# Kernel optimization log

Hardware: AMD Instinct MI355X
Metric: run time of the kernel (lower is better)

## Reference

```python
import jax, jax.numpy as jnp
import numpy as np

N, E, D, DFF, OUT = 50000, 800000, 128, 256, 119
NUM_MASK = 7500

def setup_inputs() -> dict:
    key = jax.random.key(0)
    ks = jax.random.split(key, 12)
    return {
        "x": jax.random.normal(ks[0], (N, D), jnp.float32),
        "edge_index": jax.random.randint(ks[1], (2, E), 0, N, jnp.int64),
        "edge_attr": jax.random.randint(ks[2], (E, 2), 0, 3, jnp.int64),
        "masked_idx": jax.random.randint(ks[3], (NUM_MASK,), 0, N, jnp.int64),
        "prelu_a": jnp.float32(0.25),
        "W_enc": jax.random.normal(ks[4], (D, D), jnp.float32) * (1.0 / np.sqrt(D)),
        "emb1": jax.random.normal(ks[5], (6, D), jnp.float32) * 0.1,
        "emb2": jax.random.normal(ks[6], (3, D), jnp.float32) * 0.1,
        "W1": jax.random.normal(ks[7], (DFF, D), jnp.float32) * (1.0 / np.sqrt(D)),
        "b1": jnp.zeros((DFF,), jnp.float32),
        "W2": jax.random.normal(ks[8], (OUT, DFF), jnp.float32) * (1.0 / np.sqrt(DFF)),
        "b2": jnp.zeros((OUT,), jnp.float32),
    }

def reference(x, edge_index, edge_attr, masked_idx, prelu_a, W_enc, emb1, emb2, W1, b1, W2, b2):
    n = x.shape[0]
    # PReLU -> enc_to_dec (no bias) -> zero masked nodes
    h = jnp.where(x > 0, x, prelu_a * x)
    h = h @ W_enc.T
    h = h.at[masked_idx].set(0.0)
    # add self loops (self-loop edge_attr = [4, 0])
    loop = jnp.arange(n, dtype=edge_index.dtype)
    src = jnp.concatenate([edge_index[0], loop])
    dst = jnp.concatenate([edge_index[1], loop])
    et = jnp.concatenate([edge_attr[:, 0], jnp.full((n,), 4, edge_attr.dtype)])
    ed = jnp.concatenate([edge_attr[:, 1], jnp.zeros((n,), edge_attr.dtype)])
    edge_emb = emb1[et] + emb2[ed]          # [E+N, D]
    msg = h[src] + edge_emb                 # gather + add
    aggr = jax.ops.segment_sum(msg, dst, num_segments=n)  # scatter-add
    # GIN MLP update
    hid = jax.nn.relu(aggr @ W1.T + b1)
    return hid @ W2.T + b2
```

## Files before the change

### kernel.cpp

```cpp
#include <hip/hip_runtime.h>
#include <hip/hip_fp16.h>


typedef unsigned long long ull;
typedef _Float16 half8 __attribute__((ext_vector_type(8)));
typedef float    f32x4 __attribute__((ext_vector_type(4)));

#define MFMA16(a, b, c) __builtin_amdgcn_mfma_f32_16x16x32_f16(a, b, c, 0, 0, 0)
#define BCAP 4608
#define EPB  2048

__global__ __launch_bounds__(256) void k_wconv(const float* __restrict__ Wen,
                                               const float* __restrict__ W1,
                                               const float* __restrict__ W2,
                                               __half* __restrict__ Wen16,
                                               __half* __restrict__ W1_16,
                                               __half* __restrict__ W2_16p,
                                               int* __restrict__ gcur)
{
    int i = blockIdx.x * 256 + threadIdx.x;
    if (blockIdx.x == 0) gcur[threadIdx.x] = 0;
    if (i < 128 * 128) Wen16[i] = __float2half(Wen[i]);
    if (i < 256 * 128) W1_16[i] = __float2half(W1[i]);
    if (i < 128 * 256) {
        int r = i >> 8;
        W2_16p[i] = (r < 119) ? __float2half(W2[i]) : __half(0.0f);
    }
}

__device__ __forceinline__ half8 prelu_h8(const float* __restrict__ p, float a)
{
    float4 v0 = *(const float4*)p;
    float4 v1 = *(const float4*)(p + 4);
    half8 r;
    r[0] = (_Float16)(v0.x > 0.f ? v0.x : a * v0.x);
    r[1] = (_Float16)(v0.y > 0.f ? v0.y : a * v0.y);
    r[2] = (_Float16)(v0.z > 0.f ? v0.z : a * v0.z);
    r[3] = (_Float16)(v0.w > 0.f ? v0.w : a * v0.w);
    r[4] = (_Float16)(v1.x > 0.f ? v1.x : a * v1.x);
    r[5] = (_Float16)(v1.y > 0.f ? v1.y : a * v1.y);
    r[6] = (_Float16)(v1.z > 0.f ? v1.z : a * v1.z);
    r[7] = (_Float16)(v1.w > 0.f ? v1.w : a * v1.w);
    return r;
}

__global__ __launch_bounds__(256) void k_pre(const float* __restrict__ x,
                                             const __half* __restrict__ Wen16,
                                             const float* __restrict__ prelu_a,
                                             __half* __restrict__ h16,
                                             const int* __restrict__ ei,
                                             const int* __restrict__ ea,
                                             int* __restrict__ gcur,
                                             unsigned int* __restrict__ binned,
                                             int n, int E, int nbEnc, int nbBin)
{
    __shared__ __half Wel[128 * 136];
    __shared__ int lcnt[256];
    int t = threadIdx.x;

    if ((int)blockIdx.x >= nbEnc) {
        int b = blockIdx.x - nbEnc;
        int e0 = b * EPB;
        lcnt[t] = 0;
        __syncthreads();
        unsigned int rec[8];
        int bk[8];
#pragma unroll
        for (int u = 0; u < 8; ++u) {
            int e = e0 + u * 256 + t;
            if (e < E) {
                int src = ei[e];
                int dst = ei[E + e];
                int et  = ea[2 * e];
                int ed  = ea[2 * e + 1];
                rec[u] = (unsigned int)src | ((unsigned int)et << 17)
                       | ((unsigned int)ed << 19)
                       | ((unsigned int)(dst & 255) << 21);
                bk[u] = dst >> 8;
                atomicAdd(&lcnt[bk[u]], 1);
            } else bk[u] = -1;
        }
        __syncthreads();
        int c = lcnt[t];
        lcnt[t] = (c > 0) ? atomicAdd(&gcur[t], c) : 0;
        __syncthreads();
#pragma unroll
        for (int u = 0; u < 8; ++u) {
            if (bk[u] >= 0) {
                int pos = atomicAdd(&lcnt[bk[u]], 1);
                if (pos < BCAP) binned[(size_t)bk[u] * BCAP + pos] = rec[u];
            }
        }
        return;
    }

    for (int c = t; c < 2048; c += 256) {
        int row = c >> 4, slot = c & 15;
        *(uint4*)((char*)Wel + row * 272 + slot * 16) =
            *(const uint4*)((const char*)Wen16 + (size_t)c * 16);
    }
    __syncthreads();
    int lane = t & 63, wid = t >> 6;
    int rowbase = blockIdx.x * 128 + wid * 32;
    int mr0 = min(rowbase + (lane & 15), n - 1);
    int mr1 = min(rowbase + 16 + (lane & 15), n - 1);
    int kg = (lane >> 4) * 8, slotb = lane >> 4;
    float a = prelu_a[0];
    f32x4 acc[16] = {};
#pragma unroll
    for (int ks = 0; ks < 4; ++ks) {
        half8 a0 = prelu_h8(x + ((size_t)mr0 << 7) + ks * 32 + kg, a);
        half8 a1 = prelu_h8(x + ((size_t)mr1 << 7) + ks * 32 + kg, a);
        const char* wp = (const char*)Wel + (size_t)(lane & 15) * 272
                       + (ks * 4 + slotb) * 16;
#pragma unroll
        for (int ct = 0; ct < 8; ++ct) {
            half8 bf = *(const half8*)(wp + ct * (16 * 272));
            acc[ct * 2]     = MFMA16(a0, bf, acc[ct * 2]);
            acc[ct * 2 + 1] = MFMA16(a1, bf, acc[ct * 2 + 1]);
        }
    }
#pragma unroll
    for (int ct = 0; ct < 8; ++ct)
#pragma unroll
        for (int h = 0; h < 2; ++h)
#pragma unroll
            for (int r = 0; r < 4; ++r) {
                int node = rowbase + h * 16 + ((lane >> 4) << 2) + r;
                if (node < n)
                    h16[((size_t)node << 7) + (ct << 4) + (lane & 15)] =
                        __float2half(acc[ct * 2 + h][r]);
            }
}

__global__ void k_mask(const int* __restrict__ midx,
                       unsigned int* __restrict__ h16u, int nm)
{
    int idx = blockIdx.x * blockDim.x + threadIdx.x;
    if (idx >= nm * 64) return;
    int m = idx >> 6, l = idx & 63;
    h16u[(((size_t)midx[m]) << 6) + l] = 0u;
}

__global__ __launch_bounds__(256) void k_bucket(const unsigned int* __restrict__ binned,
                                                const int* __restrict__ gcur,
                                                ull* __restrict__ cnt64,
                                                int* __restrict__ off,
                                                int* __restrict__ sorted,
                                                int n, int nb)
{
    __shared__ ull lc[256];
    __shared__ int sg[2][256];
    __shared__ int curs[256];
    int b = blockIdx.x >> 1, half = blockIdx.x & 1;
    int t = threadIdx.x;

    int gv = (t < nb) ? min(gcur[t], BCAP) : 0;
    sg[0][t] = gv;
    lc[t] = 0;
    __syncthreads();
    int cb = 0;
    for (int d = 1; d < 256; d <<= 1) {
        int v = sg[cb][t];
        if (t >= d) v += sg[cb][t - d];
        sg[cb ^ 1][t] = v;
        cb ^= 1;
        __syncthreads();
    }
    int ebase = (b == 0) ? 0 : sg[cb][b - 1];
    int mcnt = min(gcur[b], BCAP);
    __syncthreads();

    const unsigned int* bp = binned + (size_t)b * BCAP;
    for (int i = t; i < mcnt; i += 256) {
        unsigned int rec = bp[i];
        int dl = (rec >> 21) & 255;
        int et = (rec >> 17) & 3;
        int ed = (rec >> 19) & 3;
        atomicAdd(&lc[dl], (1ULL << (10 * et)) | (1ULL << (30 + 10 * ed)));
    }
    __syncthreads();

    ull c = lc[t];
    int deg = (int)((c & 1023) + ((c >> 10) & 1023) + ((c >> 20) & 1023));
    sg[0][t] = deg;
    __syncthreads();
    cb = 0;
    for (int d = 1; d < 256; d <<= 1) {
        int v = sg[cb][t];
        if (t >= d) v += sg[cb][t - d];
        sg[cb ^ 1][t] = v;
        cb ^= 1;
        __syncthreads();
    }
    int loc = sg[cb][t] - deg;
    int dst = (b << 8) + t;
    if (dst < n && (t >> 7) == half) {
        cnt64[dst] = c;
        off[dst]   = ebase + loc;
    }
    curs[t] = ebase + loc;
    __syncthreads();

    for (int i = t; i < mcnt; i += 256) {
        unsigned int rec = bp[i];
        int dl = (rec >> 21) & 255;
        if ((dl >> 7) != half) continue;
        int p = atomicAdd(&curs[dl], 1);
        sorted[p] = (int)(rec & 0x1FFFF);
    }
}

__global__ __launch_bounds__(256) void k_agg(const uint2* __restrict__ h16u2,
                                             const int* __restrict__ off,
                                             const ull* __restrict__ cnt64,
                                             const int* __restrict__ sorted,
                                             const float* __restrict__ emb1,
                                             const float* __restrict__ emb2,
                                             uint2* __restrict__ aggr16u2,
                                             int n)
{
    int t = threadIdx.x;
    int l32 = t & 31;
    int node = blockIdx.x * 8 + (t >> 5);
    if (node >= n) return;
    int p = l32 << 2;
    float4 E10 = *(const float4*)(emb1 + 0 * 128 + p);
    float4 E11 = *(const float4*)(emb1 + 1 * 128 + p);
    float4 E12 = *(const float4*)(emb1 + 2 * 128 + p);
    float4 E14 = *(const float4*)(emb1 + 4 * 128 + p);
    float4 E20 = *(const float4*)(emb2 + 0 * 128 + p);
    float4 E21 = *(const float4*)(emb2 + 1 * 128 + p);
    float4 E22 = *(const float4*)(emb2 + 2 * 128 + p);

    ull c = cnt64[node];
    float c0 = (float)(c & 1023), c1 = (float)((c >> 10) & 1023),
          c2 = (float)((c >> 20) & 1023);
    float d0 = (float)((c >> 30) & 1023), d1 = (float)((c >> 40) & 1023),
          d2 = (float)((c >> 50) & 1023);
    int deg = (int)(c & 1023) + (int)((c >> 10) & 1023) + (int)((c >> 20) & 1023);

    uint2 hv = h16u2[(size_t)node * 32 + l32];
    float2 hA = __half22float2(*(__half2*)&hv.x);
    float2 hB = __half22float2(*(__half2*)&hv.y);
    float4 base;
    base.x = hA.x + E14.x + E20.x;
    base.y = hA.y + E14.y + E20.y;
    base.z = hB.x + E14.z + E20.z;
    base.w = hB.y + E14.w + E20.w;
    base.x = fmaf(c0, E10.x, fmaf(c1, E11.x, fmaf(c2, E12.x, base.x)));
    base.y = fmaf(c0, E10.y, fmaf(c1, E11.y, fmaf(c2, E12.y, base.y)));
    base.z = fmaf(c0, E10.z, fmaf(c1, E11.z, fmaf(c2, E12.z, base.z)));
    base.w = fmaf(c0, E10.w, fmaf(c1, E11.w, fmaf(c2, E12.w, base.w)));
    base.x = fmaf(d0, E20.x, fmaf(d1, E21.x, fmaf(d2, E22.x, base.x)));
    base.y = fmaf(d0, E20.y, fmaf(d1, E21.y, fmaf(d2, E22.y, base.y)));
    base.z = fmaf(d0, E20.z, fmaf(d1, E21.z, fmaf(d2, E22.z, base.z)));
    base.w = fmaf(d0, E20.w, fmaf(d1, E21.w, fmaf(d2, E22.w, base.w)));

    __half2 aL[4], aH[4];
#pragma unroll
    for (int u = 0; u < 4; ++u) { aL[u] = __half2(); aH[u] = __half2(); }
    int i = off[node], e = i + deg;
    for (; i + 3 < e; i += 4) {
        int s0 = sorted[i],     s1 = sorted[i + 1];
        int s2 = sorted[i + 2], s3 = sorted[i + 3];
        uint2 v0 = h16u2[(size_t)s0 * 32 + l32];
        uint2 v1 = h16u2[(size_t)s1 * 32 + l32];
        uint2 v2 = h16u2[(size_t)s2 * 32 + l32];
        uint2 v3 = h16u2[(size_t)s3 * 32 + l32];
        aL[0] = __hadd2(aL[0], *(__half2*)&v0.x);
        aH[0] = __hadd2(aH[0], *(__half2*)&v0.y);
        aL[1] = __hadd2(aL[1], *(__half2*)&v1.x);
        aH[1] = __hadd2(aH[1], *(__half2*)&v1.y);
        aL[2] = __hadd2(aL[2], *(__half2*)&v2.x);
        aH[2] = __hadd2(aH[2], *(__half2*)&v2.y);
        aL[3] = __hadd2(aL[3], *(__half2*)&v3.x);
        aH[3] = __hadd2(aH[3], *(__half2*)&v3.y);
    }
    for (; i < e; ++i) {
        uint2 v0 = h16u2[(size_t)sorted[i] * 32 + l32];
        aL[0] = __hadd2(aL[0], *(__half2*)&v0.x);
        aH[0] = __hadd2(aH[0], *(__half2*)&v0.y);
    }
#pragma unroll
    for (int u = 0; u < 4; ++u) {
        float2 fL = __half22float2(aL[u]);
        float2 fH = __half22float2(aH[u]);
        base.x += fL.x; base.y += fL.y;
        base.z += fH.x; base.w += fH.y;
    }
    __half2 oL = __floats2half2_rn(base.x, base.y);
    __half2 oH = __floats2half2_rn(base.z, base.w);
    uint2 o;
    o.x = *(unsigned int*)&oL;
    o.y = *(unsigned int*)&oH;
    aggr16u2[(size_t)node * 32 + l32] = o;
}

__global__ __launch_bounds__(256, 2) void k_mlp1(const __half* __restrict__ aggr16,
                                                 const __half* __restrict__ W1_16,
                                                 const float* __restrict__ b1,
                                                 __half* __restrict__ hid16, int n)
{
    __shared__ __half Wl[256 * 136];
    int t = threadIdx.x;
    for (int c = t; c < 4096; c += 256) {
        int row = c >> 4, slot = c & 15;
        *(uint4*)((char*)Wl + row * 272 + slot * 16) =
            *(const uint4*)((const char*)W1_16 + (size_t)c * 16);
    }
    __syncthreads();
    int lane = t & 63, wid = t >> 6;
    int rowbase = blockIdx.x * 128 + wid * 32;
    int mr0 = min(rowbase + (lane & 15), n - 1);
    int mr1 = min(rowbase + 16 + (lane & 15), n - 1);
    int kg = (lane >> 4) * 8, slotb = lane >> 4;
    f32x4 acc[32] = {};
#pragma unroll
    for (int ks = 0; ks < 4; ++ks) {
        half8 a0 = *(const half8*)(aggr16 + ((size_t)mr0 << 7) + ks * 32 + kg);
        half8 a1 = *(const half8*)(aggr16 + ((size_t)mr1 << 7) + ks * 32 + kg);
        const char* wp = (const char*)Wl + (size_t)(lane & 15) * 272
                       + (ks * 4 + slotb) * 16;
#pragma unroll
        for (int ct = 0; ct < 16; ++ct) {
            half8 bf = *(const half8*)(wp + ct * (16 * 272));
            acc[ct * 2]     = MFMA16(a0, bf, acc[ct * 2]);
            acc[ct * 2 + 1] = MFMA16(a1, bf, acc[ct * 2 + 1]);
        }
    }
#pragma unroll
    for (int ct = 0; ct < 16; ++ct) {
        int col = (ct << 4) + (lane & 15);
        float bb = b1[col];
#pragma unroll
        for (int h = 0; h < 2; ++h)
#pragma unroll
            for (int r = 0; r < 4; ++r) {
                int node = rowbase + h * 16 + ((lane >> 4) << 2) + r;
                if (node < n) {
                    float v = acc[ct * 2 + h][r] + bb;
                    hid16[((size_t)node << 8) + col] =
                        __float2half(v > 0.f ? v : 0.f);
                }
            }
    }
}

__global__ __launch_bounds__(256) void k_mlp2(const __half* __restrict__ hid16,
                                              const __half* __restrict__ W2_16p,
                                              const float* __restrict__ b2,
                                              float* __restrict__ out, int n)
{
    __shared__ __half W2l[128 * 264];
    int t = threadIdx.x;
    for (int c = t; c < 4096; c += 256) {
        int row = c >> 5, slot = c & 31;
        *(uint4*)((char*)W2l + row * 528 + slot * 16) =
            *(const uint4*)((const char*)W2_16p + (size_t)c * 16);
    }
    __syncthreads();
    int lane = t & 63, wid = t >> 6;
    int rowbase = blockIdx.x * 128 + wid * 32;
    int mr0 = min(rowbase + (lane & 15), n - 1);
    int mr1 = min(rowbase + 16 + (lane & 15), n - 1);
    int kg = (lane >> 4) * 8, slotb = lane >> 4;
    f32x4 acc[16] = {};
#pragma unroll
    for (int ks = 0; ks < 8; ++ks) {
        half8 a0 = *(const half8*)(hid16 + ((size_t)mr0 << 8) + ks * 32 + kg);
        half8 a1 = *(const half8*)(hid16 + ((size_t)mr1 << 8) + ks * 32 + kg);
        const char* wp = (const char*)W2l + (size_t)(lane & 15) * 528
                       + (ks * 4 + slotb) * 16;
#pragma unroll
        for (int ct = 0; ct < 8; ++ct) {
            half8 bf = *(const half8*)(wp + ct * (16 * 528));
            acc[ct * 2]     = MFMA16(a0, bf, acc[ct * 2]);
            acc[ct * 2 + 1] = MFMA16(a1, bf, acc[ct * 2 + 1]);
        }
    }
#pragma unroll
    for (int ct = 0; ct < 8; ++ct) {
        int col = (ct << 4) + (lane & 15);
        if (col >= 119) continue;
        float bb = b2[col];
#pragma unroll
        for (int h = 0; h < 2; ++h)
#pragma unroll
            for (int r = 0; r < 4; ++r) {
                int node = rowbase + h * 16 + ((lane >> 4) << 2) + r;
                if (node < n)
                    out[(size_t)node * 119 + col] = acc[ct * 2 + h][r] + bb;
            }
    }
}

extern "C" void kernel_launch(void* const* d_in, const int* in_sizes, int n_in,
                              void* d_out, int out_size, void* d_ws, size_t ws_size,
                              hipStream_t stream)
{
    const float* x    = (const float*)d_in[0];
    const int*   ei   = (const int*)d_in[1];
    const int*   ea   = (const int*)d_in[2];
    const int*   midx = (const int*)d_in[3];
    const float* pa   = (const float*)d_in[4];
    const float* Wen  = (const float*)d_in[5];
    const float* emb1 = (const float*)d_in[6];
    const float* emb2 = (const float*)d_in[7];
    const float* W1   = (const float*)d_in[8];
    const float* b1   = (const float*)d_in[9];
    const float* W2   = (const float*)d_in[10];
    const float* b2   = (const float*)d_in[11];
    float* out = (float*)d_out;

    int n  = in_sizes[0] / 128;
    int E  = in_sizes[1] / 2;
    int nm = in_sizes[3];
    int nb = (n + 255) >> 8;

    char* ws = (char*)d_ws;
    size_t HB = (size_t)n * 128 * 2;
    __half* aggr16 = (__half*)ws;
    __half* h16    = (__half*)(ws + HB);
    __half* hid16  = (__half*)(ws + 2 * HB);
    char* p = ws + 4 * HB;
    __half* Wen16  = (__half*)p;  p += 128 * 128 * 2;
    __half* W1_16  = (__half*)p;  p += 256 * 128 * 2;
    __half* W2_16p = (__half*)p;  p += 128 * 256 * 2;
    ull* cnt64  = (ull*)p;        p += (size_t)n * 8;
    int* gcur   = (int*)p;        p += 256 * 4;
    int* off    = (int*)p;        p += (size_t)n * 4;
    int* sorted = (int*)p;        p += (size_t)E * 4;
    unsigned int* binned = (unsigned int*)p;
    p += (size_t)nb * BCAP * 4;

    int nbEnc = (n + 127) / 128;
    int nbBin = (E + EPB - 1) / EPB;

    k_wconv<<<128, 256, 0, stream>>>(Wen, W1, W2, Wen16, W1_16, W2_16p, gcur);
    k_pre  <<<nbEnc + nbBin, 256, 0, stream>>>(x, Wen16, pa, h16, ei, ea,
                                               gcur, binned, n, E, nbEnc, nbBin);
    k_mask <<<(nm * 64 + 255) / 256, 256, 0, stream>>>(midx, (unsigned int*)h16, nm);
    k_bucket<<<nb * 2, 256, 0, stream>>>(binned, gcur, cnt64, off, sorted, n, nb);
    k_agg  <<<(n + 7) / 8, 256, 0, stream>>>((const uint2*)h16, off, cnt64,
                                             sorted, emb1, emb2,
                                             (uint2*)aggr16, n);
    k_mlp1 <<<(n + 127) / 128, 256, 0, stream>>>(aggr16, W1_16, b1, hid16, n);
    k_mlp2 <<<(n + 127) / 128, 256, 0, stream>>>(hid16, W2_16p, b2, out, n);
}
```

Before: 129.7 us.

## Fold encoder matmul into W1 and move edge-embedding terms into MLP epilogue

Uses linearity to precompute Wc = W1·W_enc and per-column tables of W1 applied to the edge embeddings plus b1. The encoder GEMM is dropped and replaced by a PReLU-only elementwise fp16 pass. Aggregation now sums raw PReLU features, and the embedding count terms are added in the MLP1 epilogue through the tables. This removes one full GEMM and the per-node embedding math from the gather kernel. In exchange it adds a small serial weight-product kernel and changes fp16 rounding, since pre-encoder features are accumulated in half precision.

```diff
diff --git a/kernel.cpp b/kernel.cpp
--- a/kernel.cpp
+++ b/kernel.cpp
@@ -13,53 +13,81 @@
 __global__ __launch_bounds__(256) void k_wconv(const float* __restrict__ Wen,
                                                const float* __restrict__ W1,
                                                const float* __restrict__ W2,
-                                               __half* __restrict__ Wen16,
-                                               __half* __restrict__ W1_16,
+                                               const float* __restrict__ b1,
+                                               const float* __restrict__ emb1,
+                                               const float* __restrict__ emb2,
+                                               __half* __restrict__ Wc16,
                                                __half* __restrict__ W2_16p,
-                                               int* __restrict__ gcur)
-{
-    int i = blockIdx.x * 256 + threadIdx.x;
-    if (blockIdx.x == 0) gcur[threadIdx.x] = 0;
-    if (i < 128 * 128) Wen16[i] = __float2half(Wen[i]);
-    if (i < 256 * 128) W1_16[i] = __float2half(W1[i]);
-    if (i < 128 * 256) {
-        int r = i >> 8;
-        W2_16p[i] = (r < 119) ? __float2half(W2[i]) : __half(0.0f);
-    }
-}
-
-__device__ __forceinline__ half8 prelu_h8(const float* __restrict__ p, float a)
-{
-    float4 v0 = *(const float4*)p;
-    float4 v1 = *(const float4*)(p + 4);
-    half8 r;
-    r[0] = (_Float16)(v0.x > 0.f ? v0.x : a * v0.x);
-    r[1] = (_Float16)(v0.y > 0.f ? v0.y : a * v0.y);
-    r[2] = (_Float16)(v0.z > 0.f ? v0.z : a * v0.z);
-    r[3] = (_Float16)(v0.w > 0.f ? v0.w : a * v0.w);
-    r[4] = (_Float16)(v1.x > 0.f ? v1.x : a * v1.x);
-    r[5] = (_Float16)(v1.y > 0.f ? v1.y : a * v1.y);
-    r[6] = (_Float16)(v1.z > 0.f ? v1.z : a * v1.z);
-    r[7] = (_Float16)(v1.w > 0.f ? v1.w : a * v1.w);
-    return r;
+                                               float* __restrict__ tabs,
+                                               int* __restrict__ gcur,
+                                               int* __restrict__ off,
+                                               int n, int E)
+{
+    int b = blockIdx.x, t = threadIdx.x;
+    if (b < 128) {
+        __shared__ float We[128 * 128];
+        for (int i = t; i < 4096; i += 256) {
+            int j = i >> 5, k4 = (i & 31) << 2;
+            *(float4*)(We + (j << 7) + k4) = *(const float4*)(Wen + (j << 7) + k4);
+        }
+        __syncthreads();
+        int r = (b << 1) | (t >> 7);
+        int k = t & 127;
+        const float* w1r = W1 + ((size_t)r << 7);
+        float acc = 0.f;
+#pragma unroll 8
+        for (int j = 0; j < 128; ++j)
+            acc = fmaf(w1r[j], We[(j << 7) + k], acc);
+        Wc16[(r << 7) + k] = __float2half(acc);
+    } else if (b < 192) {
+#pragma unroll
+        for (int u = 0; u < 2; ++u) {
+            int i = (b - 128) * 512 + u * 256 + t;
+            int r = i >> 8;
+            W2_16p[i] = (r < 119) ? __float2half(W2[i]) : __half(0.0f);
+        }
+    } else if (b == 192) {
+        int col = t;
+        const float* w1r = W1 + ((size_t)col << 7);
+        float s = 0.f, t0 = 0.f, t1 = 0.f, t2 = 0.f,
+              u0 = 0.f, u1 = 0.f, u2 = 0.f;
+        for (int j = 0; j < 128; ++j) {
+            float w = w1r[j];
+            s  = fmaf(emb1[512 + j] + emb2[j], w, s);
+            t0 = fmaf(emb1[j],        w, t0);
+            t1 = fmaf(emb1[128 + j],  w, t1);
+            t2 = fmaf(emb1[256 + j],  w, t2);
+            u0 = fmaf(emb2[j],        w, u0);
+            u1 = fmaf(emb2[128 + j],  w, u1);
+            u2 = fmaf(emb2[256 + j],  w, u2);
+        }
+        tabs[col]            = s + b1[col];
+        tabs[256 + col]      = t0;
+        tabs[512 + col]      = t1;
+        tabs[768 + col]      = t2;
+        tabs[1024 + col]     = u0;
+        tabs[1280 + col]     = u1;
+        tabs[1536 + col]     = u2;
+    } else {
+        gcur[t] = 0;
+        if (t == 0) off[n] = E;
+    }
 }
 
 __global__ __launch_bounds__(256) void k_pre(const float* __restrict__ x,
-                                             const __half* __restrict__ Wen16,
                                              const float* __restrict__ prelu_a,
-                                             __half* __restrict__ h16,
+                                             uint2* __restrict__ px16u2,
                                              const int* __restrict__ ei,
                                              const int* __restrict__ ea,
                                              int* __restrict__ gcur,
                                              unsigned int* __restrict__ binned,
-                                             int n, int E, int nbEnc, int nbBin)
-{
-    __shared__ __half Wel[128 * 136];
+                                             int n, int E, int nbPx, int nbBin)
+{
     __shared__ int lcnt[256];
     int t = threadIdx.x;
 
-    if ((int)blockIdx.x >= nbEnc) {
-        int b = blockIdx.x - nbEnc;
+    if ((int)blockIdx.x >= nbPx) {
+        int b = blockIdx.x - nbPx;
         int e0 = b * EPB;
         lcnt[t] = 0;
         __syncthreads();
@@ -94,52 +122,30 @@
         return;
     }
 
-    for (int c = t; c < 2048; c += 256) {
-        int row = c >> 4, slot = c & 15;
-        *(uint4*)((char*)Wel + row * 272 + slot * 16) =
-            *(const uint4*)((const char*)Wen16 + (size_t)c * 16);
-    }
-    __syncthreads();
-    int lane = t & 63, wid = t >> 6;
-    int rowbase = blockIdx.x * 128 + wid * 32;
-    int mr0 = min(rowbase + (lane & 15), n - 1);
-    int mr1 = min(rowbase + 16 + (lane & 15), n - 1);
-    int kg = (lane >> 4) * 8, slotb = lane >> 4;
-    float a = prelu_a[0];
-    f32x4 acc[16] = {};
-#pragma unroll
-    for (int ks = 0; ks < 4; ++ks) {
-        half8 a0 = prelu_h8(x + ((size_t)mr0 << 7) + ks * 32 + kg, a);
-        half8 a1 = prelu_h8(x + ((size_t)mr1 << 7) + ks * 32 + kg, a);
-        const char* wp = (const char*)Wel + (size_t)(lane & 15) * 272
-                       + (ks * 4 + slotb) * 16;
-#pragma unroll
-        for (int ct = 0; ct < 8; ++ct) {
-            half8 bf = *(const half8*)(wp + ct * (16 * 272));
-            acc[ct * 2]     = MFMA16(a0, bf, acc[ct * 2]);
-            acc[ct * 2 + 1] = MFMA16(a1, bf, acc[ct * 2 + 1]);
-        }
-    }
-#pragma unroll
-    for (int ct = 0; ct < 8; ++ct)
-#pragma unroll
-        for (int h = 0; h < 2; ++h)
-#pragma unroll
-            for (int r = 0; r < 4; ++r) {
-                int node = rowbase + h * 16 + ((lane >> 4) << 2) + r;
-                if (node < n)
-                    h16[((size_t)node << 7) + (ct << 4) + (lane & 15)] =
-                        __float2half(acc[ct * 2 + h][r]);
-            }
+    int idx = blockIdx.x * 256 + t;
+    if (idx < n * 32) {
+        float a = prelu_a[0];
+        float4 v = *(const float4*)((const float*)x + (size_t)idx * 4);
+        v.x = v.x > 0.f ? v.x : a * v.x;
+        v.y = v.y > 0.f ? v.y : a * v.y;
+        v.z = v.z > 0.f ? v.z : a * v.z;
+        v.w = v.w > 0.f ? v.w : a * v.w;
+        __half2 lo = __floats2half2_rn(v.x, v.y);
+        __half2 hi = __floats2half2_rn(v.z, v.w);
+        uint2 o;
+        o.x = *(unsigned int*)&lo;
+        o.y = *(unsigned int*)&hi;
+        px16u2[idx] = o;
+    }
 }
 
 __global__ void k_mask(const int* __restrict__ midx,
-                       unsigned int* __restrict__ h16u, int nm)
+                       unsigned int* __restrict__ px16u, int nm)
 {
     int idx = blockIdx.x * blockDim.x + threadIdx.x;
     if (idx >= nm * 64) return;
     int m = idx >> 6, l = idx & 63;
-    h16u[(((size_t)midx[m]) << 6) + l] = 0u;
+    px16u[(((size_t)midx[m]) << 6) + l] = 0u;
 }
 
 __global__ __launch_bounds__(256) void k_bucket(const unsigned int* __restrict__ binned,
@@ -211,63 +217,32 @@
     }
 }
 
-__global__ __launch_bounds__(256) void k_agg(const uint2* __restrict__ h16u2,
+__global__ __launch_bounds__(256) void k_agg(const uint2* __restrict__ px2,
                                              const int* __restrict__ off,
-                                             const ull* __restrict__ cnt64,
                                              const int* __restrict__ sorted,
-                                             const float* __restrict__ emb1,
-                                             const float* __restrict__ emb2,
-                                             uint2* __restrict__ aggr16u2,
-                                             int n)
+                                             uint2* __restrict__ agg2, int n)
 {
     int t = threadIdx.x;
     int l32 = t & 31;
     int node = blockIdx.x * 8 + (t >> 5);
     if (node >= n) return;
-    int p = l32 << 2;
-    float4 E10 = *(const float4*)(emb1 + 0 * 128 + p);
-    float4 E11 = *(const float4*)(emb1 + 1 * 128 + p);
-    float4 E12 = *(const float4*)(emb1 + 2 * 128 + p);
-    float4 E14 = *(const float4*)(emb1 + 4 * 128 + p);
-    float4 E20 = *(const float4*)(emb2 + 0 * 128 + p);
-    float4 E21 = *(const float4*)(emb2 + 1 * 128 + p);
-    float4 E22 = *(const float4*)(emb2 + 2 * 128 + p);
-
-    ull c = cnt64[node];
-    float c0 = (float)(c & 1023), c1 = (float)((c >> 10) & 1023),
-          c2 = (float)((c >> 20) & 1023);
-    float d0 = (float)((c >> 30) & 1023), d1 = (float)((c >> 40) & 1023),
-          d2 = (float)((c >> 50) & 1023);
-    int deg = (int)(c & 1023) + (int)((c >> 10) & 1023) + (int)((c >> 20) & 1023);
-
-    uint2 hv = h16u2[(size_t)node * 32 + l32];
+
+    uint2 hv = px2[(size_t)node * 32 + l32];
     float2 hA = __half22float2(*(__half2*)&hv.x);
     float2 hB = __half22float2(*(__half2*)&hv.y);
-    float4 base;
-    base.x = hA.x + E14.x + E20.x;
-    base.y = hA.y + E14.y + E20.y;
-    base.z = hB.x + E14.z + E20.z;
-    base.w = hB.y + E14.w + E20.w;
-    base.x = fmaf(c0, E10.x, fmaf(c1, E11.x, fmaf(c2, E12.x, base.x)));
-    base.y = fmaf(c0, E10.y, fmaf(c1, E11.y, fmaf(c2, E12.y, base.y)));
-    base.z = fmaf(c0, E10.z, fmaf(c1, E11.z, fmaf(c2, E12.z, base.z)));
-    base.w = fmaf(c0, E10.w, fmaf(c1, E11.w, fmaf(c2, E12.w, base.w)));
-    base.x = fmaf(d0, E20.x, fmaf(d1, E21.x, fmaf(d2, E22.x, base.x)));
-    base.y = fmaf(d0, E20.y, fmaf(d1, E21.y, fmaf(d2, E22.y, base.y)));
-    base.z = fmaf(d0, E20.z, fmaf(d1, E21.z, fmaf(d2, E22.z, base.z)));
-    base.w = fmaf(d0, E20.w, fmaf(d1, E21.w, fmaf(d2, E22.w, base.w)));
+    float4 base = make_float4(hA.x, hA.y, hB.x, hB.y);
 
     __half2 aL[4], aH[4];
 #pragma unroll
     for (int u = 0; u < 4; ++u) { aL[u] = __half2(); aH[u] = __half2(); }
-    int i = off[node], e = i + deg;
+    int i = off[node], e = off[node + 1];
     for (; i + 3 < e; i += 4) {
         int s0 = sorted[i],     s1 = sorted[i + 1];
         int s2 = sorted[i + 2], s3 = sorted[i + 3];
-        uint2 v0 = h16u2[(size_t)s0 * 32 + l32];
-        uint2 v1 = h16u2[(size_t)s1 * 32 + l32];
-        uint2 v2 = h16u2[(size_t)s2 * 32 + l32];
-        uint2 v3 = h16u2[(size_t)s3 * 32 + l32];
+        uint2 v0 = px2[(size_t)s0 * 32 + l32];
+        uint2 v1 = px2[(size_t)s1 * 32 + l32];
+        uint2 v2 = px2[(size_t)s2 * 32 + l32];
+        uint2 v3 = px2[(size_t)s3 * 32 + l32];
         aL[0] = __hadd2(aL[0], *(__half2*)&v0.x);
         aH[0] = __hadd2(aH[0], *(__half2*)&v0.y);
         aL[1] = __hadd2(aL[1], *(__half2*)&v1.x);
@@ -278,7 +253,7 @@
         aH[3] = __hadd2(aH[3], *(__half2*)&v3.y);
     }
     for (; i < e; ++i) {
-        uint2 v0 = h16u2[(size_t)sorted[i] * 32 + l32];
+        uint2 v0 = px2[(size_t)sorted[i] * 32 + l32];
         aL[0] = __hadd2(aL[0], *(__half2*)&v0.x);
         aH[0] = __hadd2(aH[0], *(__half2*)&v0.y);
     }
@@ -294,21 +269,24 @@
     uint2 o;
     o.x = *(unsigned int*)&oL;
     o.y = *(unsigned int*)&oH;
-    aggr16u2[(size_t)node * 32 + l32] = o;
-}
-
-__global__ __launch_bounds__(256, 2) void k_mlp1(const __half* __restrict__ aggr16,
-                                                 const __half* __restrict__ W1_16,
-                                                 const float* __restrict__ b1,
+    agg2[(size_t)node * 32 + l32] = o;
+}
+
+__global__ __launch_bounds__(256, 2) void k_mlp1(const __half* __restrict__ agg16,
+                                                 const __half* __restrict__ Wc16,
+                                                 const float* __restrict__ tabs,
+                                                 const ull* __restrict__ cnt64,
                                                  __half* __restrict__ hid16, int n)
 {
     __shared__ __half Wl[256 * 136];
+    __shared__ float tl[7 * 256];
     int t = threadIdx.x;
     for (int c = t; c < 4096; c += 256) {
         int row = c >> 4, slot = c & 15;
         *(uint4*)((char*)Wl + row * 272 + slot * 16) =
-            *(const uint4*)((const char*)W1_16 + (size_t)c * 16);
-    }
+            *(const uint4*)((const char*)Wc16 + (size_t)c * 16);
+    }
+    for (int c = t; c < 1792; c += 256) tl[c] = tabs[c];
     __syncthreads();
     int lane = t & 63, wid = t >> 6;
     int rowbase = blockIdx.x * 128 + wid * 32;
@@ -318,8 +296,8 @@
     f32x4 acc[32] = {};
 #pragma unroll
     for (int ks = 0; ks < 4; ++ks) {
-        half8 a0 = *(const half8*)(aggr16 + ((size_t)mr0 << 7) + ks * 32 + kg);
-        half8 a1 = *(const half8*)(aggr16 + ((size_t)mr1 << 7) + ks * 32 + kg);
+        half8 a0 = *(const half8*)(agg16 + ((size_t)mr0 << 7) + ks * 32 + kg);
+        half8 a1 = *(const half8*)(agg16 + ((size_t)mr1 << 7) + ks * 32 + kg);
         const char* wp = (const char*)Wl + (size_t)(lane & 15) * 272
                        + (ks * 4 + slotb) * 16;
 #pragma unroll
@@ -330,20 +308,42 @@
         }
     }
 #pragma unroll
-    for (int ct = 0; ct < 16; ++ct) {
-        int col = (ct << 4) + (lane & 15);
-        float bb = b1[col];
-#pragma unroll
-        for (int h = 0; h < 2; ++h)
+    for (int h = 0; h < 2; ++h) {
+        float cf[4][6];
+        int nodes[4];
+#pragma unroll
+        for (int r = 0; r < 4; ++r) {
+            int node = rowbase + h * 16 + ((lane >> 4) << 2) + r;
+            nodes[r] = node;
+            ull c = (node < n) ? cnt64[node] : 0ULL;
+            cf[r][0] = (float)(c & 1023);
+            cf[r][1] = (float)((c >> 10) & 1023);
+            cf[r][2] = (float)((c >> 20) & 1023);
+            cf[r][3] = (float)((c >> 30) & 1023);
+            cf[r][4] = (float)((c >> 40) & 1023);
+            cf[r][5] = (float)((c >> 50) & 1023);
+        }
+#pragma unroll
+        for (int ct = 0; ct < 16; ++ct) {
+            int col = (ct << 4) + (lane & 15);
+            float S  = tl[col];
+            float T0 = tl[256 + col],  T1 = tl[512 + col],  T2 = tl[768 + col];
+            float U0 = tl[1024 + col], U1 = tl[1280 + col], U2 = tl[1536 + col];
 #pragma unroll
             for (int r = 0; r < 4; ++r) {
-                int node = rowbase + h * 16 + ((lane >> 4) << 2) + r;
-                if (node < n) {
-                    float v = acc[ct * 2 + h][r] + bb;
-                    hid16[((size_t)node << 8) + col] =
+                if (nodes[r] < n) {
+                    float v = acc[ct * 2 + h][r] + S;
+                    v = fmaf(cf[r][0], T0, v);
+                    v = fmaf(cf[r][1], T1, v);
+                    v = fmaf(cf[r][2], T2, v);
+                    v = fmaf(cf[r][3], U0, v);
+                    v = fmaf(cf[r][4], U1, v);
+                    v = fmaf(cf[r][5], U2, v);
+                    hid16[((size_t)nodes[r] << 8) + col] =
                         __float2half(v > 0.f ? v : 0.f);
                 }
             }
+        }
     }
 }
 
@@ -420,31 +420,32 @@
 
     char* ws = (char*)d_ws;
     size_t HB = (size_t)n * 128 * 2;
-    __half* aggr16 = (__half*)ws;
-    __half* h16    = (__half*)(ws + HB);
-    __half* hid16  = (__half*)(ws + 2 * HB);
+    __half* agg16 = (__half*)ws;
+    __half* px16  = (__half*)(ws + HB);
+    __half* hid16 = (__half*)(ws + 2 * HB);
     char* p = ws + 4 * HB;
-    __half* Wen16  = (__half*)p;  p += 128 * 128 * 2;
-    __half* W1_16  = (__half*)p;  p += 256 * 128 * 2;
+    __half* Wc16   = (__half*)p;  p += 256 * 128 * 2;
     __half* W2_16p = (__half*)p;  p += 128 * 256 * 2;
+    float*  tabs   = (float*)p;   p += 7 * 256 * 4;
     ull* cnt64  = (ull*)p;        p += (size_t)n * 8;
     int* gcur   = (int*)p;        p += 256 * 4;
-    int* off    = (int*)p;        p += (size_t)n * 4;
+    int* off    = (int*)p;        p += (size_t)(n + 1) * 4;
     int* sorted = (int*)p;        p += (size_t)E * 4;
     unsigned int* binned = (unsigned int*)p;
     p += (size_t)nb * BCAP * 4;
 
-    int nbEnc = (n + 127) / 128;
+    int nbPx  = (n * 32 + 255) / 256;
     int nbBin = (E + EPB - 1) / EPB;
 
-    k_wconv<<<128, 256, 0, stream>>>(Wen, W1, W2, Wen16, W1_16, W2_16p, gcur);
-    k_pre  <<<nbEnc + nbBin, 256, 0, stream>>>(x, Wen16, pa, h16, ei, ea,
-                                               gcur, binned, n, E, nbEnc, nbBin);
-    k_mask <<<(nm * 64 + 255) / 256, 256, 0, stream>>>(midx, (unsigned int*)h16, nm);
+    k_wconv<<<194, 256, 0, stream>>>(Wen, W1, W2, b1, emb1, emb2,
+                                     Wc16, W2_16p, tabs, gcur, off, n, E);
+    k_pre  <<<nbPx + nbBin, 256, 0, stream>>>(x, pa, (uint2*)px16, ei, ea,
+                                              gcur, binned, n, E, nbPx, nbBin);
+    k_mask <<<(nm * 64 + 255) / 256, 256, 0, stream>>>(midx, (unsigned int*)px16, nm);
     k_bucket<<<nb * 2, 256, 0, stream>>>(binned, gcur, cnt64, off, sorted, n, nb);
-    k_agg  <<<(n + 7) / 8, 256, 0, stream>>>((const uint2*)h16, off, cnt64,
-                                             sorted, emb1, emb2,
-                                             (uint2*)aggr16, n);
-    k_mlp1 <<<(n + 127) / 128, 256, 0, stream>>>(aggr16, W1_16, b1, hid16, n);
+    k_agg  <<<(n + 7) / 8, 256, 0, stream>>>((const uint2*)px16, off, sorted,
+                                             (uint2*)agg16, n);
+    k_mlp1 <<<(n + 127) / 128, 256, 0, stream>>>(agg16, Wc16, tabs, cnt64,
+                                                 hid16, n);
     k_mlp2 <<<(n + 127) / 128, 256, 0, stream>>>(hid16, W2_16p, b2, out, n);
 }
```

New measurement: 125.5 us. 1.03x faster.
